# Kernel tuning notes

Hardware: AMD Instinct MI355X
Metric: run time of the kernel (lower is better)

Reference implementation:

```python
import jax, jax.numpy as jnp
import numpy as np

G = 128  # voxel grid extent per axis (positions are integer voxel coords in [0, G))
K = 3    # kernel size per axis -> 27 offsets


def setup_inputs() -> dict:
    key = jax.random.key(0)
    k1, k2, k3 = jax.random.split(key, 3)
    N, Cin, Cout = 500000, 32, 32
    features = jax.random.normal(k1, (N, Cin), dtype=jnp.float32)
    in_positions = jax.random.randint(k2, (N, 3), 0, G, dtype=jnp.int32)
    # learned conv weight: one [Cin, Cout] matrix per kernel offset (27 total)
    weight = jax.random.normal(k3, (K ** 3, Cin, Cout), dtype=jnp.float32) * 0.05
    return {"features": features, "in_positions": in_positions, "weight": weight}


def _hash(pos):
    # unique linear key for integer voxel coords in [0, G)^3
    return (pos[:, 0] * G + pos[:, 1]) * G + pos[:, 2]


def reference(features, in_positions, weight):
    # Submanifold sparse conv (kernel 3x3x3, odd -> offset 0, out_positions == in_positions,
    # voxel_size = 1.0, no bias, no normalize):
    # for each active voxel, gather active neighbors at each of the 27 kernel offsets,
    # transform with the per-offset weight matrix, and accumulate.
    N = features.shape[0]
    # dense hash table: voxel key -> row index in features, -1 if inactive
    table = jnp.full((G * G * G,), -1, dtype=jnp.int32)
    table = table.at[_hash(in_positions)].set(jnp.arange(N, dtype=jnp.int32))

    out = jnp.zeros((N, weight.shape[-1]), dtype=features.dtype)
    r = K // 2
    k = 0
    for dx in range(-r, r + 1):
        for dy in range(-r, r + 1):
            for dz in range(-r, r + 1):
                npos = in_positions + jnp.array([dx, dy, dz], dtype=jnp.int32)
                inside = jnp.all((npos >= 0) & (npos < G), axis=1)
                idx = table[jnp.where(inside, _hash(npos), 0)]
                valid = inside & (idx >= 0)
                # gather active neighbor features; zero where neighbor inactive
                gathered = jnp.where(valid[:, None], features[jnp.maximum(idx, 0)], 0.0)
                out = out + gathered @ weight[k]  # [N, Cout]
                k += 1
    return out
```

## Files before the change

### kernel.cpp

```cpp
#include <hip/hip_runtime.h>


#define GRID 128
#define CIN 32
#define COUT 32
#define NOFF 27
#define NBUCKET 32768

typedef __attribute__((ext_vector_type(8))) short bf16x8;
typedef __attribute__((ext_vector_type(4))) float f32x4;

__device__ inline unsigned short f2bf(float x) {
    union { float f; unsigned u; } v; v.f = x;
    unsigned r = v.u + 0x7fff + ((v.u >> 16) & 1);
    return (unsigned short)(r >> 16);
}

__device__ inline unsigned spread3(unsigned v) {
    v &= 31u;
    v = (v | (v << 16)) & 0x030000FFu;
    v = (v | (v << 8))  & 0x0300F00Fu;
    v = (v | (v << 4))  & 0x030C30C3u;
    v = (v | (v << 2))  & 0x09249249u;
    return v;
}
__device__ inline int morton_bucket(int x, int y, int z) {
    return (int)(spread3(x >> 2) | (spread3(y >> 2) << 1) | (spread3(z >> 2) << 2));
}

__global__ void hist_kernel(const int* __restrict__ pos,
                            const float* __restrict__ wt,
                            int* __restrict__ table,
                            int* __restrict__ hist,
                            unsigned short* __restrict__ wtT, int N) {
    int i = blockIdx.x * 256 + threadIdx.x;
    if (i < N) {
        int x = pos[3 * i], y = pos[3 * i + 1], z = pos[3 * i + 2];
        int h = (x * GRID + y) * GRID + z;
        atomicMax(&table[h], i);
        atomicAdd(&hist[morton_bucket(x, y, z)], 1);
    }
    if (i < NOFF * CIN * COUT) {
        int k = i >> 10, r = i & 1023, ci = r >> 5, co = r & 31;
        wtT[k * 1024 + co * 32 + ci] = f2bf(wt[i]);
    }
}

__global__ __launch_bounds__(1024) void scan_kernel(int* __restrict__ hist) {
    __shared__ int sums[1024];
    int t = threadIdx.x;
    int base = t * 32;
    int v[32];
#pragma unroll
    for (int j = 0; j < 32; ++j) v[j] = hist[base + j];
    int s = 0;
#pragma unroll
    for (int j = 0; j < 32; ++j) { int tmp = v[j]; v[j] = s; s += tmp; }
    sums[t] = s;
    __syncthreads();
    for (int off = 1; off < 1024; off <<= 1) {
        int add = (t >= off) ? sums[t - off] : 0;
        __syncthreads();
        sums[t] += add;
        __syncthreads();
    }
    int excl = sums[t] - s;
#pragma unroll
    for (int j = 0; j < 32; ++j) hist[base + j] = excl + v[j];
}

__global__ void scatter_kernel(const int* __restrict__ pos,
                               int* __restrict__ hist,
                               int* __restrict__ table,
                               int* __restrict__ keyS,
                               int* __restrict__ origId, int N) {
    int i = blockIdx.x * 256 + threadIdx.x;
    if (i >= N) return;
    int x = pos[3 * i], y = pos[3 * i + 1], z = pos[3 * i + 2];
    int h = (x * GRID + y) * GRID + z;
    int slot = atomicAdd(&hist[morton_bucket(x, y, z)], 1);
    keyS[slot] = h;
    origId[slot] = i;
    if (table[h] == i) table[h] = -(slot + 2);
}

__global__ void convert_kernel(const float* __restrict__ feats,
                               const int* __restrict__ origId,
                               uint4* __restrict__ featsB, int N4) {
    int j = blockIdx.x * 256 + threadIdx.x;
    if (j >= N4) return;
    int slot = j >> 2, t = j & 3;
    int o = origId[slot];
    const float4* s = (const float4*)(feats + (size_t)o * CIN + t * 8);
    float4 a = s[0], b = s[1];
    uint4 r;
    r.x = (unsigned)f2bf(a.x) | ((unsigned)f2bf(a.y) << 16);
    r.y = (unsigned)f2bf(a.z) | ((unsigned)f2bf(a.w) << 16);
    r.z = (unsigned)f2bf(b.x) | ((unsigned)f2bf(b.y) << 16);
    r.w = (unsigned)f2bf(b.z) | ((unsigned)f2bf(b.w) << 16);
    featsB[j] = r;
}

__global__ __launch_bounds__(1024, 8)
void conv_kernel(const unsigned short* __restrict__ featsB,
                 const int* __restrict__ keyS,
                 const unsigned short* __restrict__ wtT,
                 const int* __restrict__ table,
                 const int* __restrict__ origId,
                 float* __restrict__ out, int N) {
    __shared__ __align__(16) unsigned short ldsw[NOFF * 1024];

    int nwg = (int)gridDim.x;
    int orig = (int)blockIdx.x;
    int q8 = nwg >> 3, r8 = nwg & 7;
    int xcd = orig & 7, lin = orig >> 3;
    int bid = (xcd < r8 ? xcd * (q8 + 1) : r8 * (q8 + 1) + (xcd - r8) * q8) + lin;

    int tid = threadIdx.x;
    int wave = tid >> 6, lane = tid & 63;
    int m = lane & 15, quad = lane >> 4;
    int tile = bid * 16 + wave;
    int base = tile * 16;
    int g = base + m;
    bool gv = g < N;

    int key = gv ? keyS[g] : 0;
    int x = key >> 14, y = (key >> 7) & 127, z = key & 127;
    bool v0[3] = {gv && x > 0, gv, gv && x < GRID - 1};
    bool v1[3] = {gv && y > 0, gv, gv && y < GRID - 1};
    bool v2[3] = {gv && z > 0, gv, gv && z < GRID - 1};

    int ids[NOFF];
#pragma unroll
    for (int k = 0; k < NOFF; ++k) {
        const int dx = k / 9, dy = (k / 3) % 3, dz = k % 3;
        bool ok = v0[dx] && v1[dy] && v2[dz];
        int hk = key + (dx - 1) * GRID * GRID + (dy - 1) * GRID + (dz - 1);
        hk = ok ? hk : 0;
        int id = table[hk];
        ids[k] = ok ? id : -1;
    }

    {
        const uint4* src = (const uint4*)wtT;
        uint4* dst = (uint4*)ldsw;
        for (int e = tid; e < NOFF * 1024 * 2 / 16; e += 1024) dst[e] = src[e];
    }
    __syncthreads();

    bf16x8 w0[NOFF], w1[NOFF];
    const unsigned short* wb = ldsw + m * 32 + quad * 8;
#pragma unroll
    for (int k = 0; k < NOFF; ++k) {
        w0[k] = *(const bf16x8*)(wb + k * 1024);
        w1[k] = *(const bf16x8*)(wb + k * 1024 + 512);
    }

    f32x4 acc0 = {0.f, 0.f, 0.f, 0.f};
    f32x4 acc1 = {0.f, 0.f, 0.f, 0.f};

#pragma unroll
    for (int k = 0; k < NOFF; ++k) {
        int id = ids[k];
        bool val = id < -1;
        int row = val ? (-id - 2) * CIN : 0;
        bf16x8 a = *(const bf16x8*)(featsB + row + quad * 8);
        if (!val) a = (bf16x8){0, 0, 0, 0, 0, 0, 0, 0};
        acc0 = __builtin_amdgcn_mfma_f32_16x16x32_bf16(a, w0[k], acc0, 0, 0, 0);
        acc1 = __builtin_amdgcn_mfma_f32_16x16x32_bf16(a, w1[k], acc1, 0, 0, 0);
    }

#pragma unroll
    for (int i = 0; i < 4; ++i) {
        int p = base + quad * 4 + i;
        if (p < N) {
            int o = origId[p];
            out[(size_t)o * COUT + m]      = acc0[i];
            out[(size_t)o * COUT + m + 16] = acc1[i];
        }
    }
}

extern "C" void kernel_launch(void* const* d_in, const int* in_sizes, int n_in,
                              void* d_out, int out_size, void* d_ws, size_t ws_size,
                              hipStream_t stream) {
    const float* feats = (const float*)d_in[0];
    const int*   pos   = (const int*)d_in[1];
    const float* wt    = (const float*)d_in[2];
    float* out = (float*)d_out;
    int N = in_sizes[0] / CIN;

    char* ws = (char*)d_ws;
    size_t off = 0;
    int* table = (int*)(ws + off);            off += (size_t)GRID * GRID * GRID * 4;
    unsigned short* wtT = (unsigned short*)(ws + off); off += 65536;
    int* hist = (int*)(ws + off);             off += NBUCKET * 4;
    int* keyS = (int*)(ws + off);             off += 2097152;
    int* origId = (int*)(ws + off);           off += 2097152;
    unsigned short* featsB = (unsigned short*)(ws + off);

    hipMemsetAsync(table, 0xFF, (size_t)GRID * GRID * GRID * 4, stream);
    hipMemsetAsync(hist, 0, NBUCKET * 4, stream);

    int blocksN = (N + 255) / 256;
    hist_kernel<<<blocksN, 256, 0, stream>>>(pos, wt, table, hist, wtT, N);
    scan_kernel<<<1, 1024, 0, stream>>>(hist);
    scatter_kernel<<<blocksN, 256, 0, stream>>>(pos, hist, table, keyS, origId, N);
    convert_kernel<<<(N * 4 + 255) / 256, 256, 0, stream>>>(feats, origId,
                                                            (uint4*)featsB, N * 4);

    int numTiles = (N + 15) / 16;
    int nwg = (numTiles + 15) / 16;
    conv_kernel<<<nwg, 1024, 0, stream>>>(featsB, keyS, wtT, table, origId, out, N);
}
```

Measured before the change: 314.5 us.

## Fuse feature conversion into scatter, wave-scan hist, pipeline gathers in conv

```diff
diff --git a/kernel.cpp b/kernel.cpp
--- a/kernel.cpp
+++ b/kernel.cpp
@@ -42,38 +42,51 @@
     }
     if (i < NOFF * CIN * COUT) {
         int k = i >> 10, r = i & 1023, ci = r >> 5, co = r & 31;
-        wtT[k * 1024 + co * 32 + ci] = f2bf(wt[i]);
+        int d = k * 1024 + (co >= 16 ? 512 : 0) + (ci >> 3) * 128 + (co & 15) * 8 + (ci & 7);
+        wtT[d] = f2bf(wt[i]);
     }
 }
 
 __global__ __launch_bounds__(1024) void scan_kernel(int* __restrict__ hist) {
-    __shared__ int sums[1024];
-    int t = threadIdx.x;
-    int base = t * 32;
-    int v[32];
-#pragma unroll
-    for (int j = 0; j < 32; ++j) v[j] = hist[base + j];
-    int s = 0;
-#pragma unroll
-    for (int j = 0; j < 32; ++j) { int tmp = v[j]; v[j] = s; s += tmp; }
-    sums[t] = s;
-    __syncthreads();
-    for (int off = 1; off < 1024; off <<= 1) {
-        int add = (t >= off) ? sums[t - off] : 0;
+    __shared__ int wsum[16];
+    int t = threadIdx.x, lane = t & 63, w = t >> 6;
+    int carry = 0;
+    for (int r = 0; r < 8; ++r) {
+        int4 v = ((int4*)hist)[r * 1024 + t];
+        int s0 = v.x, s1 = s0 + v.y, s2 = s1 + v.z, s3 = s2 + v.w;
+        int s = s3;
+        for (int off = 1; off < 64; off <<= 1) {
+            int nv = __shfl_up(s, off, 64);
+            if (lane >= off) s += nv;
+        }
+        if (lane == 63) wsum[w] = s;
         __syncthreads();
-        sums[t] += add;
+        if (w == 0) {
+            int xx = (lane < 16) ? wsum[lane] : 0;
+            for (int off = 1; off < 16; off <<= 1) {
+                int nv = __shfl_up(xx, off, 64);
+                if (lane >= off) xx += nv;
+            }
+            if (lane < 16) wsum[lane] = xx;
+        }
         __syncthreads();
-    }
-    int excl = sums[t] - s;
-#pragma unroll
-    for (int j = 0; j < 32; ++j) hist[base + j] = excl + v[j];
+        int waveExcl = (w > 0 ? wsum[w - 1] : 0);
+        int tot = wsum[15];
+        int e = carry + waveExcl + (s - s3);
+        int4 o; o.x = e; o.y = e + s0; o.z = e + s1; o.w = e + s2;
+        ((int4*)hist)[r * 1024 + t] = o;
+        carry += tot;
+        __syncthreads();
+    }
 }
 
 __global__ void scatter_kernel(const int* __restrict__ pos,
                                int* __restrict__ hist,
                                int* __restrict__ table,
                                int* __restrict__ keyS,
-                               int* __restrict__ origId, int N) {
+                               int* __restrict__ origId,
+                               const float* __restrict__ feats,
+                               unsigned short* __restrict__ featsB, int N) {
     int i = blockIdx.x * 256 + threadIdx.x;
     if (i >= N) return;
     int x = pos[3 * i], y = pos[3 * i + 1], z = pos[3 * i + 2];
@@ -82,26 +95,34 @@
     keyS[slot] = h;
     origId[slot] = i;
     if (table[h] == i) table[h] = -(slot + 2);
-}
-
-__global__ void convert_kernel(const float* __restrict__ feats,
-                               const int* __restrict__ origId,
-                               uint4* __restrict__ featsB, int N4) {
-    int j = blockIdx.x * 256 + threadIdx.x;
-    if (j >= N4) return;
-    int slot = j >> 2, t = j & 3;
-    int o = origId[slot];
-    const float4* s = (const float4*)(feats + (size_t)o * CIN + t * 8);
-    float4 a = s[0], b = s[1];
-    uint4 r;
-    r.x = (unsigned)f2bf(a.x) | ((unsigned)f2bf(a.y) << 16);
-    r.y = (unsigned)f2bf(a.z) | ((unsigned)f2bf(a.w) << 16);
-    r.z = (unsigned)f2bf(b.x) | ((unsigned)f2bf(b.y) << 16);
-    r.w = (unsigned)f2bf(b.z) | ((unsigned)f2bf(b.w) << 16);
-    featsB[j] = r;
-}
-
-__global__ __launch_bounds__(1024, 8)
+    const float4* s = (const float4*)(feats + (size_t)i * CIN);
+    uint4* d = (uint4*)(featsB + (size_t)slot * CIN);
+#pragma unroll
+    for (int j = 0; j < 4; ++j) {
+        float4 a = s[2 * j], b = s[2 * j + 1];
+        uint4 o;
+        o.x = (unsigned)f2bf(a.x) | ((unsigned)f2bf(a.y) << 16);
+        o.y = (unsigned)f2bf(a.z) | ((unsigned)f2bf(a.w) << 16);
+        o.z = (unsigned)f2bf(b.x) | ((unsigned)f2bf(b.y) << 16);
+        o.w = (unsigned)f2bf(b.z) | ((unsigned)f2bf(b.w) << 16);
+        d[j] = o;
+    }
+}
+
+#define GATHER1(dst, kk) { \
+    int r_ = rows[kk]; \
+    const unsigned short* p_ = featsB + (r_ < 0 ? 0 : r_) + quad * 8; \
+    bf16x8 t_ = *(const bf16x8*)p_; \
+    if (r_ < 0) t_ = z8; \
+    dst = t_; }
+
+#define STEP1(areg, kk) { \
+    bf16x8 b0_ = *(const bf16x8*)(wb + (kk) * 1024); \
+    bf16x8 b1_ = *(const bf16x8*)(wb + (kk) * 1024 + 512); \
+    acc0 = __builtin_amdgcn_mfma_f32_16x16x32_bf16(areg, b0_, acc0, 0, 0, 0); \
+    acc1 = __builtin_amdgcn_mfma_f32_16x16x32_bf16(areg, b1_, acc1, 0, 0, 0); }
+
+__global__ __launch_bounds__(512, 4)
 void conv_kernel(const unsigned short* __restrict__ featsB,
                  const int* __restrict__ keyS,
                  const unsigned short* __restrict__ wtT,
@@ -119,7 +140,7 @@
     int tid = threadIdx.x;
     int wave = tid >> 6, lane = tid & 63;
     int m = lane & 15, quad = lane >> 4;
-    int tile = bid * 16 + wave;
+    int tile = bid * 8 + wave;
     int base = tile * 16;
     int g = base + m;
     bool gv = g < N;
@@ -130,7 +151,7 @@
     bool v1[3] = {gv && y > 0, gv, gv && y < GRID - 1};
     bool v2[3] = {gv && z > 0, gv, gv && z < GRID - 1};
 
-    int ids[NOFF];
+    int rows[NOFF];
 #pragma unroll
     for (int k = 0; k < NOFF; ++k) {
         const int dx = k / 9, dy = (k / 3) % 3, dz = k % 3;
@@ -138,37 +159,40 @@
         int hk = key + (dx - 1) * GRID * GRID + (dy - 1) * GRID + (dz - 1);
         hk = ok ? hk : 0;
         int id = table[hk];
-        ids[k] = ok ? id : -1;
+        rows[k] = (ok && id < -1) ? (-id - 2) * CIN : -1;
     }
 
     {
         const uint4* src = (const uint4*)wtT;
         uint4* dst = (uint4*)ldsw;
-        for (int e = tid; e < NOFF * 1024 * 2 / 16; e += 1024) dst[e] = src[e];
+        for (int e = tid; e < NOFF * 1024 * 2 / 16; e += 512) dst[e] = src[e];
     }
     __syncthreads();
-
-    bf16x8 w0[NOFF], w1[NOFF];
-    const unsigned short* wb = ldsw + m * 32 + quad * 8;
-#pragma unroll
-    for (int k = 0; k < NOFF; ++k) {
-        w0[k] = *(const bf16x8*)(wb + k * 1024);
-        w1[k] = *(const bf16x8*)(wb + k * 1024 + 512);
-    }
 
     f32x4 acc0 = {0.f, 0.f, 0.f, 0.f};
     f32x4 acc1 = {0.f, 0.f, 0.f, 0.f};
-
-#pragma unroll
-    for (int k = 0; k < NOFF; ++k) {
-        int id = ids[k];
-        bool val = id < -1;
-        int row = val ? (-id - 2) * CIN : 0;
-        bf16x8 a = *(const bf16x8*)(featsB + row + quad * 8);
-        if (!val) a = (bf16x8){0, 0, 0, 0, 0, 0, 0, 0};
-        acc0 = __builtin_amdgcn_mfma_f32_16x16x32_bf16(a, w0[k], acc0, 0, 0, 0);
-        acc1 = __builtin_amdgcn_mfma_f32_16x16x32_bf16(a, w1[k], acc1, 0, 0, 0);
-    }
+    const bf16x8 z8 = {0, 0, 0, 0, 0, 0, 0, 0};
+    const unsigned short* wb = ldsw + quad * 128 + m * 8;
+
+    bf16x8 A0, A1, A2, A3, A4, A5, B0, B1, B2, B3, B4, B5;
+    GATHER1(A0, 0)  GATHER1(A1, 1)  GATHER1(A2, 2)
+    GATHER1(A3, 3)  GATHER1(A4, 4)  GATHER1(A5, 5)
+    GATHER1(B0, 6)  GATHER1(B1, 7)  GATHER1(B2, 8)
+    GATHER1(B3, 9)  GATHER1(B4, 10) GATHER1(B5, 11)
+    STEP1(A0, 0)  STEP1(A1, 1)  STEP1(A2, 2)
+    STEP1(A3, 3)  STEP1(A4, 4)  STEP1(A5, 5)
+    GATHER1(A0, 12) GATHER1(A1, 13) GATHER1(A2, 14)
+    GATHER1(A3, 15) GATHER1(A4, 16) GATHER1(A5, 17)
+    STEP1(B0, 6)  STEP1(B1, 7)  STEP1(B2, 8)
+    STEP1(B3, 9)  STEP1(B4, 10) STEP1(B5, 11)
+    GATHER1(B0, 18) GATHER1(B1, 19) GATHER1(B2, 20)
+    GATHER1(B3, 21) GATHER1(B4, 22) GATHER1(B5, 23)
+    STEP1(A0, 12) STEP1(A1, 13) STEP1(A2, 14)
+    STEP1(A3, 15) STEP1(A4, 16) STEP1(A5, 17)
+    GATHER1(A0, 24) GATHER1(A1, 25) GATHER1(A2, 26)
+    STEP1(B0, 18) STEP1(B1, 19) STEP1(B2, 20)
+    STEP1(B3, 21) STEP1(B4, 22) STEP1(B5, 23)
+    STEP1(A0, 24) STEP1(A1, 25) STEP1(A2, 26)
 
 #pragma unroll
     for (int i = 0; i < 4; ++i) {
@@ -205,11 +229,10 @@
     int blocksN = (N + 255) / 256;
     hist_kernel<<<blocksN, 256, 0, stream>>>(pos, wt, table, hist, wtT, N);
     scan_kernel<<<1, 1024, 0, stream>>>(hist);
-    scatter_kernel<<<blocksN, 256, 0, stream>>>(pos, hist, table, keyS, origId, N);
-    convert_kernel<<<(N * 4 + 255) / 256, 256, 0, stream>>>(feats, origId,
-                                                            (uint4*)featsB, N * 4);
+    scatter_kernel<<<blocksN, 256, 0, stream>>>(pos, hist, table, keyS, origId,
+                                                feats, featsB, N);
 
     int numTiles = (N + 15) / 16;
-    int nwg = (numTiles + 15) / 16;
-    conv_kernel<<<nwg, 1024, 0, stream>>>(featsB, keyS, wtT, table, origId, out, N);
-}
+    int nwg = (numTiles + 7) / 8;
+    conv_kernel<<<nwg, 512, 0, stream>>>(featsB, keyS, wtT, table, origId, out, N);
+}
```

Measured after the change: 328.3 us. +4.4%, slower.
